# Kernel tuning notes

Hardware: AMD Instinct MI355X
Metric: run time of the kernel (lower is better)

Reference implementation:

```python
import jax, jax.numpy as jnp
import numpy as np

BN_EPS = 1e-5
SMOOTH = 10.0


def l2norm(x, eps=1e-8):
    return x / (jnp.linalg.norm(x, axis=-1, keepdims=True) + eps)


def bn_tanh(z, gamma, beta):
    # BatchNorm1d in training mode (batch statistics, biased variance) + tanh
    mu = z.mean(axis=0)
    var = ((z - mu) ** 2).mean(axis=0)
    return jnp.tanh(gamma * (z - mu) / jnp.sqrt(var + BN_EPS) + beta)


def setup_inputs() -> dict:
    key = jax.random.key(0)
    ks = jax.random.split(key, 6)
    B, S, E, D = 1024, 512, 1024, 2048  # batch, att_num, embed_dim, image_dim
    return {
        "emb_instance": jax.random.normal(ks[0], (B, E), jnp.float32),
        "concept_feature": jax.random.normal(ks[1], (S, D), jnp.float32),
        "GT_label": jax.random.normal(ks[2], (B, S), jnp.float32),
        "fc1_w": jax.random.normal(ks[3], (D, E), jnp.float32) * 0.02,
        "fc1_b": jnp.zeros((E,), jnp.float32),
        "bn1_g": jnp.ones((E,), jnp.float32),
        "bn1_b": jnp.zeros((E,), jnp.float32),
        "fc2_w": jax.random.normal(ks[4], (E, E), jnp.float32) * 0.02,
        "fc2_b": jnp.zeros((E,), jnp.float32),
        "bn2_g": jnp.ones((E,), jnp.float32),
        "bn2_b": jnp.zeros((E,), jnp.float32),
        "fc3_w": jax.random.normal(ks[5], (E,), jnp.float32) * 0.02,
        "fc3_b": jnp.zeros((1,), jnp.float32),
        "GT_label_ratio": 0,
    }


def reference(emb_instance, concept_feature, GT_label, fc1_w, fc1_b, bn1_g, bn1_b,
              fc2_w, fc2_b, bn2_g, bn2_b, fc3_w, fc3_b, GT_label_ratio):
    # input_modal == 'visual' path
    W_s = bn_tanh(concept_feature @ fc1_w + fc1_b, bn1_g, bn1_b)   # (S, E)
    W_v = bn_tanh(emb_instance @ fc2_w + fc2_b, bn2_g, bn2_b)      # (B, E)
    # Fused bilinear score: fc3(W_s * W_v) == (W_v * fc3_w) @ W_s^T + fc3_b
    # avoids materializing the (B, S, E) broadcast intermediate.
    a_s = jnp.einsum('be,se->bs', W_v * fc3_w, W_s) + fc3_b        # (B, S)
    weights_v = jax.nn.softmax(a_s * SMOOTH, axis=1)
    cf = l2norm(concept_feature)                                    # (S, D)
    emb_concept = l2norm(weights_v @ cf)                            # (B, D)
    return (emb_concept, weights_v)
```

## Files before the change

kernel.cpp:

```cpp
#include <hip/hip_runtime.h>
#include <hip/hip_bf16.h>
#include <math.h>

#define B_ 1024
#define S_ 512
#define E_ 1024
#define D_ 2048
#define SMOOTH 10.0f

typedef __attribute__((ext_vector_type(8))) short bf16x8;
typedef __attribute__((ext_vector_type(4))) float f32x4;

__device__ __forceinline__ short f2bf(float f) {
    __hip_bfloat16 h = __float2bfloat16(f);
    short s; __builtin_memcpy(&s, &h, 2); return s;
}
__device__ __forceinline__ float bf2f(short s) {
    __hip_bfloat16 h; __builtin_memcpy(&h, &s, 2);
    return __bfloat162float(h);
}

__device__ __forceinline__ void gload16(const short* g, short* l) {
    __builtin_amdgcn_global_load_lds(
        (const __attribute__((address_space(1))) void*)(g),
        (__attribute__((address_space(3))) void*)(l), 16, 0, 0);
}

__inline__ __device__ float waveReduceMax(float v) {
#pragma unroll
    for (int o = 32; o; o >>= 1) v = fmaxf(v, __shfl_xor(v, o));
    return v;
}
__inline__ __device__ float waveReduceSum(float v) {
#pragma unroll
    for (int o = 32; o; o >>= 1) v += __shfl_xor(v, o);
    return v;
}

__device__ __forceinline__ void transpose_split(const float* __restrict__ in,
                                                short* __restrict__ out,
                                                int C, int r0, int c0,
                                                int ldo, int loOff,
                                                int tid, float (*t)[33]) {
    int cx = tid & 31, ry0 = tid >> 5;
#pragma unroll
    for (int i = 0; i < 4; i++) {
        int ry = ry0 + i * 8;
        t[ry][cx] = in[(size_t)(r0 + ry) * C + c0 + cx];
    }
    __syncthreads();
    int rx = tid & 31, cy0 = tid >> 5;
#pragma unroll
    for (int i = 0; i < 4; i++) {
        int cy = cy0 + i * 8;
        float v = t[rx][cy];
        size_t o = (size_t)(c0 + cy) * ldo + r0 + rx;
        short h = f2bf(v);
        out[o] = h;
        if (loOff > 0) out[o + loOff] = f2bf(v - bf2f(h));
    }
}

__global__ __launch_bounds__(256) void prep(const float* __restrict__ cf,
                                            const float* __restrict__ emb,
                                            const float* __restrict__ fc1_w,
                                            const float* __restrict__ fc2_w,
                                            short* __restrict__ A1,
                                            float* __restrict__ invn,
                                            short* __restrict__ A2,
                                            short* __restrict__ Bt1,
                                            short* __restrict__ Bt2,
                                            short* __restrict__ cfT) {
    __shared__ float t[32][33];
    __shared__ float red[4];
    const int bid = blockIdx.x;
    const int tid = threadIdx.x;
    if (bid < 512) {
        int row = bid;
        const float* x = cf + (size_t)row * D_;
        short* a = A1 + (size_t)row * (2 * D_);
        float ss = 0.f;
#pragma unroll
        for (int j = 0; j < 8; j++) {
            int i = j * 256 + tid;
            float v = x[i];
            short h = f2bf(v);
            a[i] = h;
            a[D_ + i] = f2bf(v - bf2f(h));
            ss += v * v;
        }
        ss = waveReduceSum(ss);
        if ((tid & 63) == 0) red[tid >> 6] = ss;
        __syncthreads();
        if (tid == 0) {
            float s = red[0] + red[1] + red[2] + red[3];
            invn[row] = 1.0f / (sqrtf(s) + 1e-8f);
        }
    } else if (bid < 1024) {
        int r0 = (bid - 512) * 2;
#pragma unroll
        for (int rr = 0; rr < 2; rr++) {
            int row = r0 + rr;
            const float* x = emb + (size_t)row * E_;
            short* a = A2 + (size_t)row * (2 * E_);
#pragma unroll
            for (int j = 0; j < 4; j++) {
                int i = j * 256 + tid;
                float v = x[i];
                short h = f2bf(v);
                a[i] = h;
                a[E_ + i] = f2bf(v - bf2f(h));
            }
        }
    } else if (bid < 3072) {
        int b2 = bid - 1024;
        int c0 = (b2 & 31) * 32;
        int r0 = (b2 >> 5) * 32;
        transpose_split(fc1_w, Bt1, E_, r0, c0, 2 * D_, D_, tid, t);
    } else if (bid < 4096) {
        int b2 = bid - 3072;
        int c0 = (b2 & 31) * 32;
        int r0 = (b2 >> 5) * 32;
        transpose_split(fc2_w, Bt2, E_, r0, c0, 2 * E_, E_, tid, t);
    } else {
        int b2 = bid - 4096;
        int c0 = (b2 & 63) * 32;
        int r0 = (b2 >> 6) * 32;
        transpose_split(cf, cfT, D_, r0, c0, S_, 0, tid, t);
    }
}

struct GP {
    const short* A;
    const short* Bm;
    float* P;
    int M, N, K, Kc, nx, ny;
};

__device__ __forceinline__ void gemm128_core(const GP g, int bid, short* lds) {
    const int tid = threadIdx.x;
    const int per = g.nx * g.ny;
    const int z = bid / per, rem = bid % per;
    const int by = rem / g.nx, bx = rem % g.nx;
    const int bm = by * 128, bn = bx * 128;
    const int kz = z * g.Kc;
    float* C = g.P + (size_t)z * g.M * g.N;
    const short* gA = g.A + (size_t)bm * g.K + kz;
    const short* gB = g.Bm + (size_t)bn * g.K + kz;

    size_t soff[4];
#pragma unroll
    for (int i = 0; i < 4; i++) {
        int ci = tid + i * 256;
        int row = ci >> 3, c = ci & 7;
        soff[i] = (size_t)row * g.K + ((c ^ (row & 7)) << 3);
    }

    auto stage = [&](int buf, int kt) {
        short* base = lds + buf * 16384;
#pragma unroll
        for (int i = 0; i < 4; i++) {
            gload16(gA + soff[i] + kt, base + tid * 8 + i * 2048);
            gload16(gB + soff[i] + kt, base + 8192 + tid * 8 + i * 2048);
        }
    };

    const int lane = tid & 63, wid = tid >> 6;
    const int wr = wid >> 1, wc = wid & 1;
    const int r16 = lane & 15, kg = lane >> 4;
    const int rs7 = (r16 & 7);

    f32x4 acc[4][4] = {};
    const int nt = g.Kc >> 6;

    stage(0, 0);
    for (int t = 0; t < nt; ++t) {
        __syncthreads();
        if (t + 1 < nt) stage((t + 1) & 1, (t + 1) << 6);
        const short* LA = lds + (t & 1) * 16384;
        const short* LB = LA + 8192;
#pragma unroll
        for (int ks = 0; ks < 2; ++ks) {
            const int sw = ((ks * 4 + kg) ^ rs7) << 3;
            bf16x8 a[4], b[4];
#pragma unroll
            for (int m = 0; m < 4; m++)
                a[m] = *(const bf16x8*)(LA + (wr * 64 + m * 16 + r16) * 64 + sw);
#pragma unroll
            for (int n = 0; n < 4; n++)
                b[n] = *(const bf16x8*)(LB + (wc * 64 + n * 16 + r16) * 64 + sw);
#pragma unroll
            for (int m = 0; m < 4; m++)
#pragma unroll
                for (int n = 0; n < 4; n++)
                    acc[m][n] = __builtin_amdgcn_mfma_f32_16x16x32_bf16(a[m], b[n], acc[m][n], 0, 0, 0);
        }
    }

#pragma unroll
    for (int m = 0; m < 4; m++)
#pragma unroll
        for (int n = 0; n < 4; n++) {
            int col = bn + wc * 64 + n * 16 + r16;
#pragma unroll
            for (int r = 0; r < 4; r++) {
                int row = bm + wr * 64 + m * 16 + kg * 4 + r;
                C[(size_t)row * g.N + col] = acc[m][n][r];
            }
        }
}

__global__ __launch_bounds__(256) void gemm_dual(GP g0, GP g1, int n0) {
    __shared__ short lds[32768];
    int bid = blockIdx.x;
    if (bid < n0) gemm128_core(g0, bid, lds);
    else gemm128_core(g1, bid - n0, lds);
}

__global__ __launch_bounds__(256) void gemm_one(GP g) {
    __shared__ short lds[32768];
    gemm128_core(g, blockIdx.x, lds);
}

__global__ __launch_bounds__(256) void bn_stats12(const float* __restrict__ P1,
                                                  const float* __restrict__ P2,
                                                  float* __restrict__ Z1,
                                                  float* __restrict__ Z2,
                                                  float* __restrict__ part1,
                                                  float* __restrict__ part2) {
    int c = blockIdx.x * 256 + threadIdx.x;
    if (blockIdx.y < 32) {
        int r0 = blockIdx.y * 16;
        float s = 0.f, ss = 0.f;
        for (int r = r0; r < r0 + 16; r++) {
            float z = 0.f;
#pragma unroll
            for (int k = 0; k < 4; k++) z += P1[(size_t)k * S_ * E_ + (size_t)r * E_ + c];
            Z1[(size_t)r * E_ + c] = z;
            s += z; ss += z * z;
        }
        part1[(size_t)blockIdx.y * 2 * E_ + c] = s;
        part1[(size_t)blockIdx.y * 2 * E_ + E_ + c] = ss;
    } else {
        int r0 = (blockIdx.y - 32) * 32;
        float s = 0.f, ss = 0.f;
        for (int r = r0; r < r0 + 32; r++) {
            float z = 0.f;
#pragma unroll
            for (int k = 0; k < 2; k++) z += P2[(size_t)k * B_ * E_ + (size_t)r * E_ + c];
            Z2[(size_t)r * E_ + c] = z;
            s += z; ss += z * z;
        }
        part2[(size_t)(blockIdx.y - 32) * 2 * E_ + c] = s;
        part2[(size_t)(blockIdx.y - 32) * 2 * E_ + E_ + c] = ss;
    }
}

__global__ __launch_bounds__(256) void bn_apply12(const float* __restrict__ Z1,
                                                  const float* __restrict__ Z2,
                                                  const float* __restrict__ part1,
                                                  const float* __restrict__ part2,
                                                  const float* __restrict__ g1,
                                                  const float* __restrict__ b1,
                                                  const float* __restrict__ g2,
                                                  const float* __restrict__ b2,
                                                  const float* __restrict__ fc3_w,
                                                  short* __restrict__ Ws,
                                                  short* __restrict__ Wv3) {
    int c = blockIdx.x * 256 + threadIdx.x;
    bool br1 = blockIdx.y < 32;
    const float* part = br1 ? part1 : part2;
    float s = 0.f, ss = 0.f;
#pragma unroll
    for (int k = 0; k < 32; k++) {
        s += part[(size_t)k * 2 * E_ + c];
        ss += part[(size_t)k * 2 * E_ + E_ + c];
    }
    float invR = br1 ? (1.0f / 512.0f) : (1.0f / 1024.0f);
    float mu = s * invR;
    float var = ss * invR - mu * mu;
    float rstd = rsqrtf(var + 1e-5f);
    float Aa = (br1 ? g1[c] : g2[c]) * rstd;
    float Bb = (br1 ? b1[c] : b2[c]) - Aa * mu;
    float sc = br1 ? 1.0f : fc3_w[c];
    const float* Z = br1 ? Z1 : Z2;
    short* W = br1 ? Ws : Wv3;
    int r0 = (br1 ? blockIdx.y : (blockIdx.y - 32)) * 16;
    for (int r = r0; r < r0 + 16; r++) {
        float w = tanhf(fmaf(Z[(size_t)r * E_ + c], Aa, Bb)) * sc;
        short h = f2bf(w);
        size_t o = (size_t)r * (2 * E_) + c;
        W[o] = h;
        W[o + E_] = f2bf(w - bf2f(h));
    }
}

__global__ __launch_bounds__(256) void softmax_fused(const float* __restrict__ P,
                                                     const float* __restrict__ invn,
                                                     float* __restrict__ O,
                                                     short* __restrict__ O16) {
    __shared__ float red[4];
    int row = blockIdx.x;
    int t = threadIdx.x;
    float v0 = 0.f, v1 = 0.f;
#pragma unroll
    for (int k = 0; k < 4; k++) {
        v0 += P[(size_t)k * B_ * S_ + (size_t)row * S_ + t];
        v1 += P[(size_t)k * B_ * S_ + (size_t)row * S_ + t + 256];
    }
    v0 *= SMOOTH;
    v1 *= SMOOTH;
    float m = waveReduceMax(fmaxf(v0, v1));
    if ((t & 63) == 0) red[t >> 6] = m;
    __syncthreads();
    m = fmaxf(fmaxf(red[0], red[1]), fmaxf(red[2], red[3]));
    float e0 = __expf(v0 - m), e1 = __expf(v1 - m);
    float s = waveReduceSum(e0 + e1);
    __syncthreads();
    if ((t & 63) == 0) red[t >> 6] = s;
    __syncthreads();
    s = red[0] + red[1] + red[2] + red[3];
    float inv = 1.0f / s;
    float w0 = e0 * inv, w1 = e1 * inv;
    O[(size_t)row * S_ + t] = w0;
    O[(size_t)row * S_ + t + 256] = w1;
    O16[(size_t)row * S_ + t] = f2bf(w0 * invn[t]);
    O16[(size_t)row * S_ + t + 256] = f2bf(w1 * invn[t + 256]);
}

__global__ __launch_bounds__(256) void rownorm1(const float* __restrict__ P,
                                                float* __restrict__ O) {
    __shared__ float red[4];
    int row = blockIdx.x;
    int t = threadIdx.x;
    float v[8];
    float ss = 0.f;
#pragma unroll
    for (int j = 0; j < 8; j++) {
        v[j] = P[(size_t)row * D_ + j * 256 + t];
        ss += v[j] * v[j];
    }
    ss = waveReduceSum(ss);
    if ((t & 63) == 0) red[t >> 6] = ss;
    __syncthreads();
    ss = red[0] + red[1] + red[2] + red[3];
    float sc = 1.0f / (sqrtf(ss) + 1e-8f);
#pragma unroll
    for (int j = 0; j < 8; j++)
        O[(size_t)row * D_ + j * 256 + t] = v[j] * sc;
}

extern "C" void kernel_launch(void* const* d_in, const int* in_sizes, int n_in,
                              void* d_out, int out_size, void* d_ws, size_t ws_size,
                              hipStream_t stream) {
    const float* emb   = (const float*)d_in[0];
    const float* cf    = (const float*)d_in[1];
    const float* fc1_w = (const float*)d_in[3];
    const float* bn1_g = (const float*)d_in[5];
    const float* bn1_b = (const float*)d_in[6];
    const float* fc2_w = (const float*)d_in[7];
    const float* bn2_g = (const float*)d_in[9];
    const float* bn2_b = (const float*)d_in[10];
    const float* fc3_w = (const float*)d_in[11];

    float* out = (float*)d_out;
    float* emb_concept = out;
    float* weights_v   = out + (size_t)B_ * D_;

    const size_t MB = 1024 * 1024;
    char* w = (char*)d_ws;
    short* Bt1  = (short*)(w + 0 * MB);
    short* A1   = (short*)(w + 8 * MB);
    short* A2   = (short*)(w + 12 * MB);
    short* Bt2  = (short*)(w + 16 * MB);
    short* cfT  = (short*)(w + 20 * MB);
    float* Z1   = (float*)(w + 22 * MB);
    float* Z2   = (float*)(w + 24 * MB);
    short* Ws   = (short*)(w + 28 * MB);
    short* Wv3  = (short*)(w + 30 * MB);
    short* A4   = (short*)(w + 34 * MB);
    float* part1 = (float*)(w + 35 * MB);
    float* part2 = (float*)(w + 36 * MB);
    float* invn  = (float*)(w + 37 * MB);
    float* P1   = (float*)(w + 40 * MB);
    float* P2   = (float*)(w + 48 * MB);
    float* P3   = (float*)(w + 40 * MB);
    float* emb_pre = (float*)(w + 48 * MB);

    prep<<<5120, 256, 0, stream>>>(cf, emb, fc1_w, fc2_w, A1, invn, A2, Bt1, Bt2, cfT);

    GP g1 = {A1, Bt1, P1, S_, E_, 2 * D_, 1024, 8, 4};
    GP g2 = {A2, Bt2, P2, B_, E_, 2 * E_, 1024, 8, 8};
    gemm_dual<<<256, 256, 0, stream>>>(g1, g2, 128);

    bn_stats12<<<dim3(4, 64), 256, 0, stream>>>(P1, P2, Z1, Z2, part1, part2);
    bn_apply12<<<dim3(4, 96), 256, 0, stream>>>(Z1, Z2, part1, part2, bn1_g, bn1_b,
                                                bn2_g, bn2_b, fc3_w, Ws, Wv3);

    GP g3 = {Wv3, Ws, P3, B_, S_, 2 * E_, 512, 4, 8};
    gemm_one<<<128, 256, 0, stream>>>(g3);

    softmax_fused<<<B_, 256, 0, stream>>>(P3, invn, weights_v, A4);

    GP g4 = {A4, cfT, emb_pre, B_, D_, S_, 512, 16, 8};
    gemm_one<<<128, 256, 0, stream>>>(g4);

    rownorm1<<<B_, 256, 0, stream>>>(emb_pre, emb_concept);
}
```

Measured before the change: 71.54 us.

## Drop bf16 hi/lo split emulation, use single bf16 operands for GEMMs

Removes the two-term bf16 split (hi plus residual lo) that doubled the K dimension of the fc1, fc2 and score GEMMs. Now each operand is a single bf16 value, which halves the GEMM K-work, the prep writes and the workspace traffic. The change also packs kernel arguments into a struct and compacts the workspace layout. The risk is accuracy: bf16-only products may lose precision relative to the fp32 reference, especially in the softmax scores scaled by 10.

```diff
diff --git a/kernel.cpp b/kernel.cpp
--- a/kernel.cpp
+++ b/kernel.cpp
@@ -15,10 +15,6 @@
     __hip_bfloat16 h = __float2bfloat16(f);
     short s; __builtin_memcpy(&s, &h, 2); return s;
 }
-__device__ __forceinline__ float bf2f(short s) {
-    __hip_bfloat16 h; __builtin_memcpy(&h, &s, 2);
-    return __bfloat162float(h);
-}
 
 __device__ __forceinline__ void gload16(const short* g, short* l) {
     __builtin_amdgcn_global_load_lds(
@@ -37,11 +33,17 @@
     return v;
 }
 
-__device__ __forceinline__ void transpose_split(const float* __restrict__ in,
-                                                short* __restrict__ out,
-                                                int C, int r0, int c0,
-                                                int ldo, int loOff,
-                                                int tid, float (*t)[33]) {
+struct KArgs {
+    const float *cf, *emb, *fc1w, *fc2w, *bn1g, *bn1b, *bn2g, *bn2b, *fc3w;
+    short *A1, *A2, *Bt1, *Bt2, *cfT, *Ws, *Wv3, *A4;
+    float *invn, *Z1, *Z2, *part1, *part2, *P1, *P2, *P3, *emb_pre;
+    float *weights_v, *emb_concept;
+};
+
+__device__ __forceinline__ void transpose_bf(const float* __restrict__ in,
+                                             short* __restrict__ out,
+                                             int C, int r0, int c0, int ldo,
+                                             int tid, float (*t)[33]) {
     int cx = tid & 31, ry0 = tid >> 5;
 #pragma unroll
     for (int i = 0; i < 4; i++) {
@@ -53,40 +55,25 @@
 #pragma unroll
     for (int i = 0; i < 4; i++) {
         int cy = cy0 + i * 8;
-        float v = t[rx][cy];
-        size_t o = (size_t)(c0 + cy) * ldo + r0 + rx;
-        short h = f2bf(v);
-        out[o] = h;
-        if (loOff > 0) out[o + loOff] = f2bf(v - bf2f(h));
-    }
-}
-
-__global__ __launch_bounds__(256) void prep(const float* __restrict__ cf,
-                                            const float* __restrict__ emb,
-                                            const float* __restrict__ fc1_w,
-                                            const float* __restrict__ fc2_w,
-                                            short* __restrict__ A1,
-                                            float* __restrict__ invn,
-                                            short* __restrict__ A2,
-                                            short* __restrict__ Bt1,
-                                            short* __restrict__ Bt2,
-                                            short* __restrict__ cfT) {
+        out[(size_t)(c0 + cy) * ldo + r0 + rx] = f2bf(t[rx][cy]);
+    }
+}
+
+__global__ __launch_bounds__(256) void prep_k(KArgs a) {
     __shared__ float t[32][33];
     __shared__ float red[4];
-    const int bid = blockIdx.x;
+    const int task = blockIdx.x;
     const int tid = threadIdx.x;
-    if (bid < 512) {
-        int row = bid;
-        const float* x = cf + (size_t)row * D_;
-        short* a = A1 + (size_t)row * (2 * D_);
+    if (task < 512) {
+        int row = task;
+        const float* x = a.cf + (size_t)row * D_;
+        short* aa = a.A1 + (size_t)row * D_;
         float ss = 0.f;
 #pragma unroll
         for (int j = 0; j < 8; j++) {
             int i = j * 256 + tid;
             float v = x[i];
-            short h = f2bf(v);
-            a[i] = h;
-            a[D_ + i] = f2bf(v - bf2f(h));
+            aa[i] = f2bf(v);
             ss += v * v;
         }
         ss = waveReduceSum(ss);
@@ -94,39 +81,36 @@
         __syncthreads();
         if (tid == 0) {
             float s = red[0] + red[1] + red[2] + red[3];
-            invn[row] = 1.0f / (sqrtf(s) + 1e-8f);
-        }
-    } else if (bid < 1024) {
-        int r0 = (bid - 512) * 2;
+            a.invn[row] = 1.0f / (sqrtf(s) + 1e-8f);
+        }
+    } else if (task < 1024) {
+        int r0 = (task - 512) * 2;
 #pragma unroll
         for (int rr = 0; rr < 2; rr++) {
             int row = r0 + rr;
-            const float* x = emb + (size_t)row * E_;
-            short* a = A2 + (size_t)row * (2 * E_);
+            const float* x = a.emb + (size_t)row * E_;
+            short* aa = a.A2 + (size_t)row * E_;
 #pragma unroll
             for (int j = 0; j < 4; j++) {
                 int i = j * 256 + tid;
-                float v = x[i];
-                short h = f2bf(v);
-                a[i] = h;
-                a[E_ + i] = f2bf(v - bf2f(h));
+                aa[i] = f2bf(x[i]);
             }
         }
-    } else if (bid < 3072) {
-        int b2 = bid - 1024;
+    } else if (task < 3072) {
+        int b2 = task - 1024;
         int c0 = (b2 & 31) * 32;
         int r0 = (b2 >> 5) * 32;
-        transpose_split(fc1_w, Bt1, E_, r0, c0, 2 * D_, D_, tid, t);
-    } else if (bid < 4096) {
-        int b2 = bid - 3072;
+        transpose_bf(a.fc1w, a.Bt1, E_, r0, c0, D_, tid, t);
+    } else if (task < 4096) {
+        int b2 = task - 3072;
         int c0 = (b2 & 31) * 32;
         int r0 = (b2 >> 5) * 32;
-        transpose_split(fc2_w, Bt2, E_, r0, c0, 2 * E_, E_, tid, t);
+        transpose_bf(a.fc2w, a.Bt2, E_, r0, c0, E_, tid, t);
     } else {
-        int b2 = bid - 4096;
+        int b2 = task - 4096;
         int c0 = (b2 & 63) * 32;
         int r0 = (b2 >> 6) * 32;
-        transpose_split(cf, cfT, D_, r0, c0, S_, 0, tid, t);
+        transpose_bf(a.cf, a.cfT, D_, r0, c0, S_, tid, t);
     }
 }
 
@@ -222,12 +206,7 @@
     gemm128_core(g, blockIdx.x, lds);
 }
 
-__global__ __launch_bounds__(256) void bn_stats12(const float* __restrict__ P1,
-                                                  const float* __restrict__ P2,
-                                                  float* __restrict__ Z1,
-                                                  float* __restrict__ Z2,
-                                                  float* __restrict__ part1,
-                                                  float* __restrict__ part2) {
+__global__ __launch_bounds__(256) void bn_stats12(KArgs a) {
     int c = blockIdx.x * 256 + threadIdx.x;
     if (blockIdx.y < 32) {
         int r0 = blockIdx.y * 16;
@@ -235,41 +214,32 @@
         for (int r = r0; r < r0 + 16; r++) {
             float z = 0.f;
 #pragma unroll
-            for (int k = 0; k < 4; k++) z += P1[(size_t)k * S_ * E_ + (size_t)r * E_ + c];
-            Z1[(size_t)r * E_ + c] = z;
+            for (int k = 0; k < 4; k++) z += a.P1[(size_t)k * S_ * E_ + (size_t)r * E_ + c];
+            a.Z1[(size_t)r * E_ + c] = z;
             s += z; ss += z * z;
         }
-        part1[(size_t)blockIdx.y * 2 * E_ + c] = s;
-        part1[(size_t)blockIdx.y * 2 * E_ + E_ + c] = ss;
+        a.part1[(size_t)blockIdx.y * 2 * E_ + c] = s;
+        a.part1[(size_t)blockIdx.y * 2 * E_ + E_ + c] = ss;
     } else {
-        int r0 = (blockIdx.y - 32) * 32;
+        int y2 = blockIdx.y - 32;
+        int r0 = y2 * 32;
         float s = 0.f, ss = 0.f;
         for (int r = r0; r < r0 + 32; r++) {
             float z = 0.f;
 #pragma unroll
-            for (int k = 0; k < 2; k++) z += P2[(size_t)k * B_ * E_ + (size_t)r * E_ + c];
-            Z2[(size_t)r * E_ + c] = z;
+            for (int k = 0; k < 2; k++) z += a.P2[(size_t)k * B_ * E_ + (size_t)r * E_ + c];
+            a.Z2[(size_t)r * E_ + c] = z;
             s += z; ss += z * z;
         }
-        part2[(size_t)(blockIdx.y - 32) * 2 * E_ + c] = s;
-        part2[(size_t)(blockIdx.y - 32) * 2 * E_ + E_ + c] = ss;
-    }
-}
-
-__global__ __launch_bounds__(256) void bn_apply12(const float* __restrict__ Z1,
-                                                  const float* __restrict__ Z2,
-                                                  const float* __restrict__ part1,
-                                                  const float* __restrict__ part2,
-                                                  const float* __restrict__ g1,
-                                                  const float* __restrict__ b1,
-                                                  const float* __restrict__ g2,
-                                                  const float* __restrict__ b2,
-                                                  const float* __restrict__ fc3_w,
-                                                  short* __restrict__ Ws,
-                                                  short* __restrict__ Wv3) {
+        a.part2[(size_t)y2 * 2 * E_ + c] = s;
+        a.part2[(size_t)y2 * 2 * E_ + E_ + c] = ss;
+    }
+}
+
+__global__ __launch_bounds__(256) void bn_apply12(KArgs a) {
     int c = blockIdx.x * 256 + threadIdx.x;
     bool br1 = blockIdx.y < 32;
-    const float* part = br1 ? part1 : part2;
+    const float* part = br1 ? a.part1 : a.part2;
     float s = 0.f, ss = 0.f;
 #pragma unroll
     for (int k = 0; k < 32; k++) {
@@ -280,130 +250,123 @@
     float mu = s * invR;
     float var = ss * invR - mu * mu;
     float rstd = rsqrtf(var + 1e-5f);
-    float Aa = (br1 ? g1[c] : g2[c]) * rstd;
-    float Bb = (br1 ? b1[c] : b2[c]) - Aa * mu;
-    float sc = br1 ? 1.0f : fc3_w[c];
-    const float* Z = br1 ? Z1 : Z2;
-    short* W = br1 ? Ws : Wv3;
-    int r0 = (br1 ? blockIdx.y : (blockIdx.y - 32)) * 16;
-    for (int r = r0; r < r0 + 16; r++) {
+    float Aa = (br1 ? a.bn1g[c] : a.bn2g[c]) * rstd;
+    float Bb = (br1 ? a.bn1b[c] : a.bn2b[c]) - Aa * mu;
+    float sc = br1 ? 1.0f : a.fc3w[c];
+    const float* Z = br1 ? a.Z1 : a.Z2;
+    short* W = br1 ? a.Ws : a.Wv3;
+    int nr = br1 ? 16 : 32;
+    int r0 = (br1 ? blockIdx.y : (blockIdx.y - 32)) * nr;
+    for (int r = r0; r < r0 + nr; r++) {
         float w = tanhf(fmaf(Z[(size_t)r * E_ + c], Aa, Bb)) * sc;
-        short h = f2bf(w);
-        size_t o = (size_t)r * (2 * E_) + c;
-        W[o] = h;
-        W[o + E_] = f2bf(w - bf2f(h));
-    }
-}
-
-__global__ __launch_bounds__(256) void softmax_fused(const float* __restrict__ P,
-                                                     const float* __restrict__ invn,
-                                                     float* __restrict__ O,
-                                                     short* __restrict__ O16) {
+        W[(size_t)r * E_ + c] = f2bf(w);
+    }
+}
+
+__global__ __launch_bounds__(256) void softmax_k(KArgs a) {
     __shared__ float red[4];
     int row = blockIdx.x;
-    int t = threadIdx.x;
+    int tid = threadIdx.x;
     float v0 = 0.f, v1 = 0.f;
 #pragma unroll
     for (int k = 0; k < 4; k++) {
-        v0 += P[(size_t)k * B_ * S_ + (size_t)row * S_ + t];
-        v1 += P[(size_t)k * B_ * S_ + (size_t)row * S_ + t + 256];
+        v0 += a.P3[(size_t)k * B_ * S_ + (size_t)row * S_ + tid];
+        v1 += a.P3[(size_t)k * B_ * S_ + (size_t)row * S_ + tid + 256];
     }
     v0 *= SMOOTH;
     v1 *= SMOOTH;
     float m = waveReduceMax(fmaxf(v0, v1));
-    if ((t & 63) == 0) red[t >> 6] = m;
+    if ((tid & 63) == 0) red[tid >> 6] = m;
     __syncthreads();
     m = fmaxf(fmaxf(red[0], red[1]), fmaxf(red[2], red[3]));
     float e0 = __expf(v0 - m), e1 = __expf(v1 - m);
     float s = waveReduceSum(e0 + e1);
     __syncthreads();
-    if ((t & 63) == 0) red[t >> 6] = s;
+    if ((tid & 63) == 0) red[tid >> 6] = s;
     __syncthreads();
     s = red[0] + red[1] + red[2] + red[3];
     float inv = 1.0f / s;
     float w0 = e0 * inv, w1 = e1 * inv;
-    O[(size_t)row * S_ + t] = w0;
-    O[(size_t)row * S_ + t + 256] = w1;
-    O16[(size_t)row * S_ + t] = f2bf(w0 * invn[t]);
-    O16[(size_t)row * S_ + t + 256] = f2bf(w1 * invn[t + 256]);
-}
-
-__global__ __launch_bounds__(256) void rownorm1(const float* __restrict__ P,
-                                                float* __restrict__ O) {
+    a.weights_v[(size_t)row * S_ + tid] = w0;
+    a.weights_v[(size_t)row * S_ + tid + 256] = w1;
+    a.A4[(size_t)row * S_ + tid] = f2bf(w0 * a.invn[tid]);
+    a.A4[(size_t)row * S_ + tid + 256] = f2bf(w1 * a.invn[tid + 256]);
+}
+
+__global__ __launch_bounds__(256) void rownorm_k(KArgs a) {
     __shared__ float red[4];
     int row = blockIdx.x;
-    int t = threadIdx.x;
+    int tid = threadIdx.x;
     float v[8];
     float ss = 0.f;
 #pragma unroll
     for (int j = 0; j < 8; j++) {
-        v[j] = P[(size_t)row * D_ + j * 256 + t];
+        v[j] = a.emb_pre[(size_t)row * D_ + j * 256 + tid];
         ss += v[j] * v[j];
     }
     ss = waveReduceSum(ss);
-    if ((t & 63) == 0) red[t >> 6] = ss;
+    if ((tid & 63) == 0) red[tid >> 6] = ss;
     __syncthreads();
     ss = red[0] + red[1] + red[2] + red[3];
     float sc = 1.0f / (sqrtf(ss) + 1e-8f);
 #pragma unroll
     for (int j = 0; j < 8; j++)
-        O[(size_t)row * D_ + j * 256 + t] = v[j] * sc;
+        a.emb_concept[(size_t)row * D_ + j * 256 + tid] = v[j] * sc;
 }
 
 extern "C" void kernel_launch(void* const* d_in, const int* in_sizes, int n_in,
                               void* d_out, int out_size, void* d_ws, size_t ws_size,
                               hipStream_t stream) {
-    const float* emb   = (const float*)d_in[0];
-    const float* cf    = (const float*)d_in[1];
-    const float* fc1_w = (const float*)d_in[3];
-    const float* bn1_g = (const float*)d_in[5];
-    const float* bn1_b = (const float*)d_in[6];
-    const float* fc2_w = (const float*)d_in[7];
-    const float* bn2_g = (const float*)d_in[9];
-    const float* bn2_b = (const float*)d_in[10];
-    const float* fc3_w = (const float*)d_in[11];
-
     float* out = (float*)d_out;
-    float* emb_concept = out;
-    float* weights_v   = out + (size_t)B_ * D_;
-
     const size_t MB = 1024 * 1024;
     char* w = (char*)d_ws;
-    short* Bt1  = (short*)(w + 0 * MB);
-    short* A1   = (short*)(w + 8 * MB);
-    short* A2   = (short*)(w + 12 * MB);
-    short* Bt2  = (short*)(w + 16 * MB);
-    short* cfT  = (short*)(w + 20 * MB);
-    float* Z1   = (float*)(w + 22 * MB);
-    float* Z2   = (float*)(w + 24 * MB);
-    short* Ws   = (short*)(w + 28 * MB);
-    short* Wv3  = (short*)(w + 30 * MB);
-    short* A4   = (short*)(w + 34 * MB);
-    float* part1 = (float*)(w + 35 * MB);
-    float* part2 = (float*)(w + 36 * MB);
-    float* invn  = (float*)(w + 37 * MB);
-    float* P1   = (float*)(w + 40 * MB);
-    float* P2   = (float*)(w + 48 * MB);
-    float* P3   = (float*)(w + 40 * MB);
-    float* emb_pre = (float*)(w + 48 * MB);
-
-    prep<<<5120, 256, 0, stream>>>(cf, emb, fc1_w, fc2_w, A1, invn, A2, Bt1, Bt2, cfT);
-
-    GP g1 = {A1, Bt1, P1, S_, E_, 2 * D_, 1024, 8, 4};
-    GP g2 = {A2, Bt2, P2, B_, E_, 2 * E_, 1024, 8, 8};
+
+    KArgs a;
+    a.cf   = (const float*)d_in[1];
+    a.emb  = (const float*)d_in[0];
+    a.fc1w = (const float*)d_in[3];
+    a.fc2w = (const float*)d_in[7];
+    a.bn1g = (const float*)d_in[5];
+    a.bn1b = (const float*)d_in[6];
+    a.bn2g = (const float*)d_in[9];
+    a.bn2b = (const float*)d_in[10];
+    a.fc3w = (const float*)d_in[11];
+    a.Bt1  = (short*)(w + 0 * MB);
+    a.Bt2  = (short*)(w + 4 * MB);
+    a.A1   = (short*)(w + 6 * MB);
+    a.A2   = (short*)(w + 8 * MB);
+    a.cfT  = (short*)(w + 10 * MB);
+    a.Z1   = (float*)(w + 12 * MB);
+    a.Z2   = (float*)(w + 14 * MB);
+    a.Ws   = (short*)(w + 18 * MB);
+    a.Wv3  = (short*)(w + 19 * MB);
+    a.A4   = (short*)(w + 21 * MB);
+    a.part1 = (float*)(w + 22 * MB);
+    a.part2 = (float*)(w + 22 * MB + 512 * 1024);
+    a.invn  = (float*)(w + 23 * MB);
+    a.P1   = (float*)(w + 24 * MB);
+    a.P2   = (float*)(w + 32 * MB);
+    a.P3   = (float*)(w + 24 * MB);
+    a.emb_pre = (float*)(w + 32 * MB);
+    a.emb_concept = out;
+    a.weights_v   = out + (size_t)B_ * D_;
+
+    prep_k<<<5120, 256, 0, stream>>>(a);
+
+    GP g1 = {a.A1, a.Bt1, a.P1, S_, E_, D_, 512, 8, 4};
+    GP g2 = {a.A2, a.Bt2, a.P2, B_, E_, E_, 512, 8, 8};
     gemm_dual<<<256, 256, 0, stream>>>(g1, g2, 128);
 
-    bn_stats12<<<dim3(4, 64), 256, 0, stream>>>(P1, P2, Z1, Z2, part1, part2);
-    bn_apply12<<<dim3(4, 96), 256, 0, stream>>>(Z1, Z2, part1, part2, bn1_g, bn1_b,
-                                                bn2_g, bn2_b, fc3_w, Ws, Wv3);
-
-    GP g3 = {Wv3, Ws, P3, B_, S_, 2 * E_, 512, 4, 8};
+    bn_stats12<<<dim3(4, 64), 256, 0, stream>>>(a);
+    bn_apply12<<<dim3(4, 64), 256, 0, stream>>>(a);
+
+    GP g3 = {a.Wv3, a.Ws, a.P3, B_, S_, E_, 256, 4, 8};
     gemm_one<<<128, 256, 0, stream>>>(g3);
 
-    softmax_fused<<<B_, 256, 0, stream>>>(P3, invn, weights_v, A4);
-
-    GP g4 = {A4, cfT, emb_pre, B_, D_, S_, 512, 16, 8};
+    softmax_k<<<B_, 256, 0, stream>>>(a);
+
+    GP g4 = {a.A4, a.cfT, a.emb_pre, B_, D_, S_, 512, 16, 8};
     gemm_one<<<128, 256, 0, stream>>>(g4);
 
-    rownorm1<<<B_, 256, 0, stream>>>(emb_pre, emb_concept);
-}
+    rownorm_k<<<B_, 256, 0, stream>>>(a);
+}
```

Result: slower. 74.80 us (+4.6%).
